# Kernel optimization log

Hardware: AMD Instinct MI355X
Metric: run time of the kernel (lower is better)

The kernel has to match this reference:

```python
import jax, jax.numpy as jnp
import numpy as np

N_EMBD = 1024
NUM_EXPERTS = 8
TOP_K = 2


def new_gelu(x):
    # NewGELU: tanh approximation used by GPT-2
    c = jnp.sqrt(2.0 / jnp.pi).astype(x.dtype)
    return 0.5 * x * (1.0 + jnp.tanh(c * (x + 0.044715 * x ** 3)))


def setup_inputs() -> dict:
    key = jax.random.key(0)
    ks = jax.random.split(key, 6)
    C, E, H = N_EMBD, NUM_EXPERTS, 4 * N_EMBD
    x = jax.random.normal(ks[0], (4, 2048, C), dtype=jnp.float32)
    router_w = 0.02 * jax.random.normal(ks[1], (E, C), dtype=jnp.float32)  # Linear(C,E,bias=False).weight
    w1 = 0.02 * jax.random.normal(ks[2], (E, H, C), dtype=jnp.float32)     # c_fc.weight per expert
    b1 = jnp.zeros((E, H), dtype=jnp.float32)
    w2 = 0.02 * jax.random.normal(ks[3], (E, C, H), dtype=jnp.float32)     # c_proj.weight per expert
    b2 = jnp.zeros((E, C), dtype=jnp.float32)
    return {"x": x, "router_w": router_w, "w1": w1, "b1": b1, "w2": w2, "b2": b2}


def reference(x, router_w, w1, b1, w2, b2):
    B, T, C = x.shape
    E = router_w.shape[0]
    x_flat = x.reshape(B * T, C)  # [N, C]

    router_logits = x_flat @ router_w.T              # [N, E]
    router_probs = jax.nn.softmax(router_logits, axis=-1)
    top_k_probs, top_k_idx = jax.lax.top_k(router_probs, TOP_K)  # [N, K]
    top_k_probs = top_k_probs / (top_k_probs.sum(axis=-1, keepdims=True) + 1e-8)

    # combine weights per (token, expert): sum over k of gate_k * onehot(idx_k)
    cw = (jax.nn.one_hot(top_k_idx, E, dtype=x.dtype) * top_k_probs[..., None]).sum(axis=1)  # [N, E]

    output = jnp.zeros_like(x_flat)
    for e in range(E):  # small fixed expert count
        h = new_gelu(x_flat @ w1[e].T + b1[e])       # [N, 4C]
        out_e = h @ w2[e].T + b2[e]                  # [N, C]
        output = output + cw[:, e:e + 1] * out_e

    return output.reshape(B, T, C)
```

## Files before the change

### kernel.cpp

```cpp
#include <hip/hip_runtime.h>
#include <hip/hip_bf16.h>
#include <math.h>


#define N_TOK   8192
#define C_DIM   1024
#define H_DIM   4096
#define N_EXP   8
#define CAP     8192

typedef __bf16 bf16;
typedef bf16  bf16x8 __attribute__((ext_vector_type(8)));
typedef float f32x4  __attribute__((ext_vector_type(4)));

__device__ __forceinline__ void async_ld16(const void* g, void* l) {
    __builtin_amdgcn_global_load_lds(
        (const __attribute__((address_space(1))) void*)g,
        (__attribute__((address_space(3))) void*)l,
        16, 0, 0);
}

__device__ __forceinline__ float gelu_f(float v) {
    float u = v + 0.044715f * v * v * v;
    return 0.5f * v * (1.0f + tanhf(0.7978845608028654f * u));
}

__global__ void cvt_k(const float* __restrict__ src, bf16* __restrict__ dst, int n8) {
    int i = blockIdx.x * blockDim.x + threadIdx.x;
    if (i >= n8) return;
    const float4* p = (const float4*)src + (size_t)i * 2;
    float4 a = p[0], b = p[1];
    bf16x8 v;
    v[0] = (bf16)a.x; v[1] = (bf16)a.y; v[2] = (bf16)a.z; v[3] = (bf16)a.w;
    v[4] = (bf16)b.x; v[5] = (bf16)b.y; v[6] = (bf16)b.z; v[7] = (bf16)b.w;
    *((bf16x8*)dst + i) = v;
}

__global__ __launch_bounds__(1024) void router_k(const float* __restrict__ x,
                                                 const float* __restrict__ rw,
                                                 int* __restrict__ counts,
                                                 int* __restrict__ tok,
                                                 float* __restrict__ gate) {
    __shared__ int lcnt[N_EXP];
    __shared__ int lbase[N_EXP];
    const int tid  = threadIdx.x;
    const int lane = tid & 63;
    const int wv   = tid >> 6;
    if (tid < N_EXP) lcnt[tid] = 0;
    __syncthreads();

    const int t = blockIdx.x * 16 + wv;

    float dot[N_EXP];
#pragma unroll
    for (int e = 0; e < N_EXP; ++e) dot[e] = 0.f;
    const float4* xr = (const float4*)(x + (size_t)t * C_DIM);
#pragma unroll
    for (int j = 0; j < 4; ++j) {
        float4 xv = xr[j * 64 + lane];
#pragma unroll
        for (int e = 0; e < N_EXP; ++e) {
            float4 w4 = ((const float4*)(rw + (size_t)e * C_DIM))[j * 64 + lane];
            dot[e] += xv.x * w4.x + xv.y * w4.y + xv.z * w4.z + xv.w * w4.w;
        }
    }
#pragma unroll
    for (int e = 0; e < N_EXP; ++e) {
#pragma unroll
        for (int o = 32; o > 0; o >>= 1) dot[e] += __shfl_xor(dot[e], o, 64);
    }

    int a = 0, b = 0, ra = 0, rb = 0;
    float g0 = 0.f, g1 = 0.f;
    if (lane == 0) {
        float m = dot[0];
#pragma unroll
        for (int e = 1; e < N_EXP; ++e) m = fmaxf(m, dot[e]);
        float p[N_EXP]; float s = 0.f;
#pragma unroll
        for (int e = 0; e < N_EXP; ++e) { p[e] = expf(dot[e] - m); s += p[e]; }
        a = 0;
#pragma unroll
        for (int e = 1; e < N_EXP; ++e) if (p[e] > p[a]) a = e;
        b = -1;
#pragma unroll
        for (int e = 0; e < N_EXP; ++e) if (e != a && (b < 0 || p[e] > p[b])) b = e;
        float pa = p[a] / s, pb = p[b] / s;
        float d = pa + pb + 1e-8f;
        g0 = pa / d; g1 = pb / d;
        ra = atomicAdd(&lcnt[a], 1);
        rb = atomicAdd(&lcnt[b], 1);
    }
    __syncthreads();
    if (tid < N_EXP) lbase[tid] = atomicAdd(&counts[tid], lcnt[tid]);
    __syncthreads();
    if (lane == 0) {
        int sa = lbase[a] + ra;
        int sb = lbase[b] + rb;
        tok[a * CAP + sa] = t;  gate[a * CAP + sa] = g0;
        tok[b * CAP + sb] = t;  gate[b * CAP + sb] = g1;
    }
}

__global__ void prefix_k(const int* __restrict__ counts, int* __restrict__ offs) {
    if (threadIdx.x == 0) {
        int s = 0;
        for (int e = 0; e < N_EXP; ++e) { offs[e] = s; s += counts[e]; }
    }
}


__global__ __launch_bounds__(256) void fc1_k(const bf16* __restrict__ xb,
                                             const bf16* __restrict__ w1b,
                                             const float* __restrict__ b1,
                                             const int* __restrict__ counts,
                                             const int* __restrict__ offs,
                                             const int* __restrict__ tok,
                                             bf16* __restrict__ h) {
    const int e   = blockIdx.z;
    const int cnt = counts[e];
    const int m0  = blockIdx.y * 128;
    if (m0 >= cnt) return;
    const int n0  = blockIdx.x * 128;
    const int off = offs[e];

    __shared__ __align__(16) bf16 As[128][32];
    __shared__ __align__(16) bf16 Bs[128][32];

    const int tid  = threadIdx.x;
    const int lane = tid & 63;
    const int wv   = tid >> 6;
    const int wm   = wv & 1;
    const int wn   = wv >> 1;

    const int scol = (((lane & 3) ^ ((lane >> 3) & 3))) * 8;

    const int ar0 = wv * 16 + (lane >> 2);
    const int ar1 = 64 + wv * 16 + (lane >> 2);
    const int i0 = m0 + ar0, i1 = m0 + ar1;
    const int t0 = tok[e * CAP + (i0 < cnt ? i0 : cnt - 1)];
    const int t1 = tok[e * CAP + (i1 < cnt ? i1 : cnt - 1)];
    const bf16* ga0 = xb + (size_t)t0 * C_DIM + scol;
    const bf16* ga1 = xb + (size_t)t1 * C_DIM + scol;
    bf16* la0 = &As[wv * 16][0];
    bf16* la1 = &As[64 + wv * 16][0];

    const bf16* gb0 = w1b + ((size_t)e * H_DIM + n0 + ar0) * C_DIM + scol;
    const bf16* gb1 = w1b + ((size_t)e * H_DIM + n0 + ar1) * C_DIM + scol;
    bf16* lb0 = &Bs[wv * 16][0];
    bf16* lb1 = &Bs[64 + wv * 16][0];

    f32x4 acc[4][4];
#pragma unroll
    for (int mi = 0; mi < 4; ++mi)
#pragma unroll
        for (int ni = 0; ni < 4; ++ni)
#pragma unroll
            for (int r = 0; r < 4; ++r) acc[mi][ni][r] = 0.f;

    const int r_   = lane & 15;
    const int g_   = lane >> 4;
    const int rcol = (g_ ^ ((r_ >> 1) & 3)) * 8;

    for (int kt = 0; kt < C_DIM / 32; ++kt) {
        const int k0 = kt * 32;
        async_ld16(ga0 + k0, la0);
        async_ld16(ga1 + k0, la1);
        async_ld16(gb0 + k0, lb0);
        async_ld16(gb1 + k0, lb1);
        __syncthreads();

        bf16x8 af[4];
#pragma unroll
        for (int mi = 0; mi < 4; ++mi)
            af[mi] = *(const bf16x8*)&As[wm * 64 + mi * 16 + r_][rcol];
#pragma unroll
        for (int ni = 0; ni < 4; ++ni) {
            bf16x8 bfr = *(const bf16x8*)&Bs[wn * 64 + ni * 16 + r_][rcol];
#pragma unroll
            for (int mi = 0; mi < 4; ++mi)
                acc[mi][ni] = __builtin_amdgcn_mfma_f32_16x16x32_bf16(af[mi], bfr, acc[mi][ni], 0, 0, 0);
        }
        __syncthreads();
    }

    const int lg = lane >> 4, ln = lane & 15;
#pragma unroll
    for (int mi = 0; mi < 4; ++mi) {
#pragma unroll
        for (int r = 0; r < 4; ++r) {
            const int m = wm * 64 + mi * 16 + lg * 4 + r;
            if (m0 + m < cnt) {
                const size_t hrow = (size_t)(off + m0 + m) * H_DIM;
#pragma unroll
                for (int ni = 0; ni < 4; ++ni) {
                    const int n = n0 + wn * 64 + ni * 16 + ln;
                    float v = acc[mi][ni][r] + b1[(size_t)e * H_DIM + n];
                    h[hrow + n] = (bf16)gelu_f(v);
                }
            }
        }
    }
}

__global__ __launch_bounds__(256) void fc2_k(const bf16* __restrict__ h,
                                             const bf16* __restrict__ w2b,
                                             const float* __restrict__ b2,
                                             const int* __restrict__ counts,
                                             const int* __restrict__ offs,
                                             const int* __restrict__ tok,
                                             const float* __restrict__ gate,
                                             float* __restrict__ out) {
    const int e   = blockIdx.z;
    const int cnt = counts[e];
    const int m0  = blockIdx.y * 128;
    if (m0 >= cnt) return;
    const int n0  = blockIdx.x * 128;
    const int off = offs[e];

    __shared__ __align__(16) bf16 As[128][32];
    __shared__ __align__(16) bf16 Bs[128][32];

    const int tid  = threadIdx.x;
    const int lane = tid & 63;
    const int wv   = tid >> 6;
    const int wm   = wv & 1;
    const int wn   = wv >> 1;

    const int scol = (((lane & 3) ^ ((lane >> 3) & 3))) * 8;

    const int ar0 = wv * 16 + (lane >> 2);
    const int ar1 = 64 + wv * 16 + (lane >> 2);
    const int i0 = m0 + ar0, i1 = m0 + ar1;
    const size_t hr0 = (size_t)(off + (i0 < cnt ? i0 : cnt - 1)) * H_DIM;
    const size_t hr1 = (size_t)(off + (i1 < cnt ? i1 : cnt - 1)) * H_DIM;
    const bf16* ga0 = h + hr0 + scol;
    const bf16* ga1 = h + hr1 + scol;
    bf16* la0 = &As[wv * 16][0];
    bf16* la1 = &As[64 + wv * 16][0];

    const bf16* gb0 = w2b + ((size_t)e * C_DIM + n0 + ar0) * H_DIM + scol;
    const bf16* gb1 = w2b + ((size_t)e * C_DIM + n0 + ar1) * H_DIM + scol;
    bf16* lb0 = &Bs[wv * 16][0];
    bf16* lb1 = &Bs[64 + wv * 16][0];

    f32x4 acc[4][4];
#pragma unroll
    for (int mi = 0; mi < 4; ++mi)
#pragma unroll
        for (int ni = 0; ni < 4; ++ni)
#pragma unroll
            for (int r = 0; r < 4; ++r) acc[mi][ni][r] = 0.f;

    const int r_   = lane & 15;
    const int g_   = lane >> 4;
    const int rcol = (g_ ^ ((r_ >> 1) & 3)) * 8;

    for (int kt = 0; kt < H_DIM / 32; ++kt) {
        const int k0 = kt * 32;
        async_ld16(ga0 + k0, la0);
        async_ld16(ga1 + k0, la1);
        async_ld16(gb0 + k0, lb0);
        async_ld16(gb1 + k0, lb1);
        __syncthreads();

        bf16x8 af[4];
#pragma unroll
        for (int mi = 0; mi < 4; ++mi)
            af[mi] = *(const bf16x8*)&As[wm * 64 + mi * 16 + r_][rcol];
#pragma unroll
        for (int ni = 0; ni < 4; ++ni) {
            bf16x8 bfr = *(const bf16x8*)&Bs[wn * 64 + ni * 16 + r_][rcol];
#pragma unroll
            for (int mi = 0; mi < 4; ++mi)
                acc[mi][ni] = __builtin_amdgcn_mfma_f32_16x16x32_bf16(af[mi], bfr, acc[mi][ni], 0, 0, 0);
        }
        __syncthreads();
    }

    const int lg = lane >> 4, ln = lane & 15;
#pragma unroll
    for (int mi = 0; mi < 4; ++mi) {
#pragma unroll
        for (int r = 0; r < 4; ++r) {
            const int m = wm * 64 + mi * 16 + lg * 4 + r;
            if (m0 + m < cnt) {
                const int   tk = tok[e * CAP + m0 + m];
                const float g  = gate[e * CAP + m0 + m];
#pragma unroll
                for (int ni = 0; ni < 4; ++ni) {
                    const int n = n0 + wn * 64 + ni * 16 + ln;
                    float v = (acc[mi][ni][r] + b2[(size_t)e * C_DIM + n]) * g;
                    atomicAdd(&out[(size_t)tk * C_DIM + n], v);
                }
            }
        }
    }
}

extern "C" void kernel_launch(void* const* d_in, const int* in_sizes, int n_in,
                              void* d_out, int out_size, void* d_ws, size_t ws_size,
                              hipStream_t stream) {
    const float* x  = (const float*)d_in[0];
    const float* rw = (const float*)d_in[1];
    const float* w1 = (const float*)d_in[2];
    const float* b1 = (const float*)d_in[3];
    const float* w2 = (const float*)d_in[4];
    const float* b2 = (const float*)d_in[5];
    float* out = (float*)d_out;

    char* ws = (char*)d_ws;
    size_t o = 0;
    bf16* xb     = (bf16*)(ws + o);  o += (size_t)N_TOK * C_DIM * sizeof(bf16);
    bf16* w1b    = (bf16*)(ws + o);  o += (size_t)N_EXP * H_DIM * C_DIM * sizeof(bf16);
    bf16* w2b    = (bf16*)(ws + o);  o += (size_t)N_EXP * C_DIM * H_DIM * sizeof(bf16);
    int*  tok    = (int*)(ws + o);   o += (size_t)N_EXP * CAP * sizeof(int);
    float* gate  = (float*)(ws + o); o += (size_t)N_EXP * CAP * sizeof(float);
    int*  counts = (int*)(ws + o);   o += 128;
    int*  offs   = (int*)(ws + o);   o += 128;
    bf16* h      = (bf16*)(ws + o);  o += (size_t)(2 * N_TOK) * H_DIM * sizeof(bf16);

    hipMemsetAsync(d_out, 0, (size_t)N_TOK * C_DIM * sizeof(float), stream);
    hipMemsetAsync(counts, 0, 128, stream);

    const int NW = N_EXP * H_DIM * C_DIM / 8;
    cvt_k<<<dim3((N_TOK * C_DIM / 8 + 255) / 256), 256, 0, stream>>>(x, xb, N_TOK * C_DIM / 8);
    cvt_k<<<dim3((NW + 255) / 256), 256, 0, stream>>>(w1, w1b, NW);
    cvt_k<<<dim3((NW + 255) / 256), 256, 0, stream>>>(w2, w2b, NW);
    router_k<<<dim3(N_TOK / 16), dim3(1024), 0, stream>>>(x, rw, counts, tok, gate);
    prefix_k<<<dim3(1), dim3(64), 0, stream>>>(counts, offs);
    fc1_k<<<dim3(H_DIM / 128, N_TOK / 128, N_EXP), dim3(256), 0, stream>>>(xb, w1b, b1, counts, offs, tok, h);
    fc2_k<<<dim3(C_DIM / 128, N_TOK / 128, N_EXP), dim3(256), 0, stream>>>(h, w2b, b2, counts, offs, tok, gate, out);
}
```

Baseline: 908.5 us.

## Double K-tile depth to 64 and remap grid for XCD-aware block scheduling

Measured after the change: 908.8 us. No clear change (+0.0%).

```diff
diff --git a/kernel.cpp b/kernel.cpp
--- a/kernel.cpp
+++ b/kernel.cpp
@@ -117,15 +117,21 @@
                                              const int* __restrict__ offs,
                                              const int* __restrict__ tok,
                                              bf16* __restrict__ h) {
-    const int e   = blockIdx.z;
-    const int cnt = counts[e];
-    const int m0  = blockIdx.y * 128;
+    const int bid  = blockIdx.x;
+    const int slot = bid & 7;
+    const int inner = bid >> 3;
+    const int xB   = inner & 31;
+    const int yL   = inner >> 5;
+    const int yG   = yL * 8 + slot;
+    const int e    = yG >> 6;
+    const int m0   = (yG & 63) * 128;
+    const int cnt  = counts[e];
     if (m0 >= cnt) return;
-    const int n0  = blockIdx.x * 128;
-    const int off = offs[e];
-
-    __shared__ __align__(16) bf16 As[128][32];
-    __shared__ __align__(16) bf16 Bs[128][32];
+    const int n0   = xB * 128;
+    const int off  = offs[e];
+
+    __shared__ __align__(16) bf16 As[128][64];
+    __shared__ __align__(16) bf16 Bs[128][64];
 
     const int tid  = threadIdx.x;
     const int lane = tid & 63;
@@ -133,22 +139,20 @@
     const int wm   = wv & 1;
     const int wn   = wv >> 1;
 
-    const int scol = (((lane & 3) ^ ((lane >> 3) & 3))) * 8;
-
-    const int ar0 = wv * 16 + (lane >> 2);
-    const int ar1 = 64 + wv * 16 + (lane >> 2);
-    const int i0 = m0 + ar0, i1 = m0 + ar1;
-    const int t0 = tok[e * CAP + (i0 < cnt ? i0 : cnt - 1)];
-    const int t1 = tok[e * CAP + (i1 < cnt ? i1 : cnt - 1)];
-    const bf16* ga0 = xb + (size_t)t0 * C_DIM + scol;
-    const bf16* ga1 = xb + (size_t)t1 * C_DIM + scol;
-    bf16* la0 = &As[wv * 16][0];
-    bf16* la1 = &As[64 + wv * 16][0];
-
-    const bf16* gb0 = w1b + ((size_t)e * H_DIM + n0 + ar0) * C_DIM + scol;
-    const bf16* gb1 = w1b + ((size_t)e * H_DIM + n0 + ar1) * C_DIM + scol;
-    bf16* lb0 = &Bs[wv * 16][0];
-    bf16* lb1 = &Bs[64 + wv * 16][0];
+    const int swz  = (((lane >> 3) & 1) << 2) | (lane >> 4);
+    const int scol = ((lane & 7) ^ swz) * 8;
+    const int rbase = wv * 8 + (lane >> 3);
+
+    const bf16* gA[4]; const bf16* gB[4];
+#pragma unroll
+    for (int p = 0; p < 4; ++p) {
+        const int i = m0 + p * 32 + rbase;
+        const int t = tok[e * CAP + (i < cnt ? i : cnt - 1)];
+        gA[p] = xb + (size_t)t * C_DIM + scol;
+        gB[p] = w1b + ((size_t)e * H_DIM + n0 + p * 32 + rbase) * C_DIM + scol;
+    }
+    char* ldsA = (char*)&As[0][0] + (size_t)(wv * 8) * 128 + (size_t)lane * 16;
+    char* ldsB = (char*)&Bs[0][0] + (size_t)(wv * 8) * 128 + (size_t)lane * 16;
 
     f32x4 acc[4][4];
 #pragma unroll
@@ -158,28 +162,35 @@
 #pragma unroll
             for (int r = 0; r < 4; ++r) acc[mi][ni][r] = 0.f;
 
-    const int r_   = lane & 15;
-    const int g_   = lane >> 4;
-    const int rcol = (g_ ^ ((r_ >> 1) & 3)) * 8;
-
-    for (int kt = 0; kt < C_DIM / 32; ++kt) {
-        const int k0 = kt * 32;
-        async_ld16(ga0 + k0, la0);
-        async_ld16(ga1 + k0, la1);
-        async_ld16(gb0 + k0, lb0);
-        async_ld16(gb1 + k0, lb1);
+    const int r_ = lane & 15;
+    const int g_ = lane >> 4;
+    const int fr = ((r_ & 1) << 2) | ((r_ >> 1) & 3);
+    const int col0 = ((g_)     ^ fr) * 8;
+    const int col1 = ((4 + g_) ^ fr) * 8;
+
+    for (int kt = 0; kt < C_DIM / 64; ++kt) {
+        const int k0 = kt * 64;
+#pragma unroll
+        for (int p = 0; p < 4; ++p) {
+            async_ld16(gA[p] + k0, ldsA + p * 4096);
+            async_ld16(gB[p] + k0, ldsB + p * 4096);
+        }
         __syncthreads();
 
-        bf16x8 af[4];
-#pragma unroll
-        for (int mi = 0; mi < 4; ++mi)
-            af[mi] = *(const bf16x8*)&As[wm * 64 + mi * 16 + r_][rcol];
-#pragma unroll
-        for (int ni = 0; ni < 4; ++ni) {
-            bf16x8 bfr = *(const bf16x8*)&Bs[wn * 64 + ni * 16 + r_][rcol];
+#pragma unroll
+        for (int s = 0; s < 2; ++s) {
+            const int cc = s ? col1 : col0;
+            bf16x8 af[4];
 #pragma unroll
             for (int mi = 0; mi < 4; ++mi)
-                acc[mi][ni] = __builtin_amdgcn_mfma_f32_16x16x32_bf16(af[mi], bfr, acc[mi][ni], 0, 0, 0);
+                af[mi] = *(const bf16x8*)&As[wm * 64 + mi * 16 + r_][cc];
+#pragma unroll
+            for (int ni = 0; ni < 4; ++ni) {
+                bf16x8 bfr = *(const bf16x8*)&Bs[wn * 64 + ni * 16 + r_][cc];
+#pragma unroll
+                for (int mi = 0; mi < 4; ++mi)
+                    acc[mi][ni] = __builtin_amdgcn_mfma_f32_16x16x32_bf16(af[mi], bfr, acc[mi][ni], 0, 0, 0);
+            }
         }
         __syncthreads();
     }
@@ -211,15 +222,21 @@
                                              const int* __restrict__ tok,
                                              const float* __restrict__ gate,
                                              float* __restrict__ out) {
-    const int e   = blockIdx.z;
-    const int cnt = counts[e];
-    const int m0  = blockIdx.y * 128;
+    const int bid  = blockIdx.x;
+    const int slot = bid & 7;
+    const int inner = bid >> 3;
+    const int xB   = inner & 7;
+    const int yL   = inner >> 3;
+    const int yG   = yL * 8 + slot;
+    const int e    = yG >> 6;
+    const int m0   = (yG & 63) * 128;
+    const int cnt  = counts[e];
     if (m0 >= cnt) return;
-    const int n0  = blockIdx.x * 128;
-    const int off = offs[e];
-
-    __shared__ __align__(16) bf16 As[128][32];
-    __shared__ __align__(16) bf16 Bs[128][32];
+    const int n0   = xB * 128;
+    const int off  = offs[e];
+
+    __shared__ __align__(16) bf16 As[128][64];
+    __shared__ __align__(16) bf16 Bs[128][64];
 
     const int tid  = threadIdx.x;
     const int lane = tid & 63;
@@ -227,22 +244,19 @@
     const int wm   = wv & 1;
     const int wn   = wv >> 1;
 
-    const int scol = (((lane & 3) ^ ((lane >> 3) & 3))) * 8;
-
-    const int ar0 = wv * 16 + (lane >> 2);
-    const int ar1 = 64 + wv * 16 + (lane >> 2);
-    const int i0 = m0 + ar0, i1 = m0 + ar1;
-    const size_t hr0 = (size_t)(off + (i0 < cnt ? i0 : cnt - 1)) * H_DIM;
-    const size_t hr1 = (size_t)(off + (i1 < cnt ? i1 : cnt - 1)) * H_DIM;
-    const bf16* ga0 = h + hr0 + scol;
-    const bf16* ga1 = h + hr1 + scol;
-    bf16* la0 = &As[wv * 16][0];
-    bf16* la1 = &As[64 + wv * 16][0];
-
-    const bf16* gb0 = w2b + ((size_t)e * C_DIM + n0 + ar0) * H_DIM + scol;
-    const bf16* gb1 = w2b + ((size_t)e * C_DIM + n0 + ar1) * H_DIM + scol;
-    bf16* lb0 = &Bs[wv * 16][0];
-    bf16* lb1 = &Bs[64 + wv * 16][0];
+    const int swz  = (((lane >> 3) & 1) << 2) | (lane >> 4);
+    const int scol = ((lane & 7) ^ swz) * 8;
+    const int rbase = wv * 8 + (lane >> 3);
+
+    const bf16* gA[4]; const bf16* gB[4];
+#pragma unroll
+    for (int p = 0; p < 4; ++p) {
+        const int i = m0 + p * 32 + rbase;
+        gA[p] = h + (size_t)(off + (i < cnt ? i : cnt - 1)) * H_DIM + scol;
+        gB[p] = w2b + ((size_t)e * C_DIM + n0 + p * 32 + rbase) * H_DIM + scol;
+    }
+    char* ldsA = (char*)&As[0][0] + (size_t)(wv * 8) * 128 + (size_t)lane * 16;
+    char* ldsB = (char*)&Bs[0][0] + (size_t)(wv * 8) * 128 + (size_t)lane * 16;
 
     f32x4 acc[4][4];
 #pragma unroll
@@ -252,28 +266,35 @@
 #pragma unroll
             for (int r = 0; r < 4; ++r) acc[mi][ni][r] = 0.f;
 
-    const int r_   = lane & 15;
-    const int g_   = lane >> 4;
-    const int rcol = (g_ ^ ((r_ >> 1) & 3)) * 8;
-
-    for (int kt = 0; kt < H_DIM / 32; ++kt) {
-        const int k0 = kt * 32;
-        async_ld16(ga0 + k0, la0);
-        async_ld16(ga1 + k0, la1);
-        async_ld16(gb0 + k0, lb0);
-        async_ld16(gb1 + k0, lb1);
+    const int r_ = lane & 15;
+    const int g_ = lane >> 4;
+    const int fr = ((r_ & 1) << 2) | ((r_ >> 1) & 3);
+    const int col0 = ((g_)     ^ fr) * 8;
+    const int col1 = ((4 + g_) ^ fr) * 8;
+
+    for (int kt = 0; kt < H_DIM / 64; ++kt) {
+        const int k0 = kt * 64;
+#pragma unroll
+        for (int p = 0; p < 4; ++p) {
+            async_ld16(gA[p] + k0, ldsA + p * 4096);
+            async_ld16(gB[p] + k0, ldsB + p * 4096);
+        }
         __syncthreads();
 
-        bf16x8 af[4];
-#pragma unroll
-        for (int mi = 0; mi < 4; ++mi)
-            af[mi] = *(const bf16x8*)&As[wm * 64 + mi * 16 + r_][rcol];
-#pragma unroll
-        for (int ni = 0; ni < 4; ++ni) {
-            bf16x8 bfr = *(const bf16x8*)&Bs[wn * 64 + ni * 16 + r_][rcol];
+#pragma unroll
+        for (int s = 0; s < 2; ++s) {
+            const int cc = s ? col1 : col0;
+            bf16x8 af[4];
 #pragma unroll
             for (int mi = 0; mi < 4; ++mi)
-                acc[mi][ni] = __builtin_amdgcn_mfma_f32_16x16x32_bf16(af[mi], bfr, acc[mi][ni], 0, 0, 0);
+                af[mi] = *(const bf16x8*)&As[wm * 64 + mi * 16 + r_][cc];
+#pragma unroll
+            for (int ni = 0; ni < 4; ++ni) {
+                bf16x8 bfr = *(const bf16x8*)&Bs[wn * 64 + ni * 16 + r_][cc];
+#pragma unroll
+                for (int mi = 0; mi < 4; ++mi)
+                    acc[mi][ni] = __builtin_amdgcn_mfma_f32_16x16x32_bf16(af[mi], bfr, acc[mi][ni], 0, 0, 0);
+            }
         }
         __syncthreads();
     }
@@ -329,6 +350,6 @@
     cvt_k<<<dim3((NW + 255) / 256), 256, 0, stream>>>(w2, w2b, NW);
     router_k<<<dim3(N_TOK / 16), dim3(1024), 0, stream>>>(x, rw, counts, tok, gate);
     prefix_k<<<dim3(1), dim3(64), 0, stream>>>(counts, offs);
-    fc1_k<<<dim3(H_DIM / 128, N_TOK / 128, N_EXP), dim3(256), 0, stream>>>(xb, w1b, b1, counts, offs, tok, h);
-    fc2_k<<<dim3(C_DIM / 128, N_TOK / 128, N_EXP), dim3(256), 0, stream>>>(h, w2b, b2, counts, offs, tok, gate, out);
-}
+    fc1_k<<<dim3(32 * 64 * N_EXP), dim3(256), 0, stream>>>(xb, w1b, b1, counts, offs, tok, h);
+    fc2_k<<<dim3(8 * 64 * N_EXP), dim3(256), 0, stream>>>(h, w2b, b2, counts, offs, tok, gate, out);
+}
```
